# Kernel optimization log

Measured on AMD Instinct MI355X. Metric: run time of the kernel, lower is better.

## Reference

```python
import jax, jax.numpy as jnp
import numpy as np

N_INPUTS = 128
N_LATENT = 21
LEN_TIME = 51
NUM_SHIFTS = 50
BATCH = 2048
N_HIDDEN = 4  # hidden relu layers in the outer DenseResBlock


def setup_inputs() -> dict:
    key = jax.random.key(0)
    ks = jax.random.split(key, 8)
    s = 0.05  # small init scale keeps activations sane through the residual stack
    return {
        "inputs": jax.random.normal(ks[0], (BATCH, LEN_TIME, N_INPUTS), jnp.float32),
        "L": jnp.eye(N_LATENT, dtype=jnp.float32)
             + s * jax.random.normal(ks[1], (N_LATENT, N_LATENT), jnp.float32),
        "ienc_W": s * jax.random.normal(ks[2], (N_INPUTS, N_LATENT), jnp.float32),
        "idec_W": s * jax.random.normal(ks[3], (N_LATENT, N_INPUTS), jnp.float32),
        "enc_W": s * jax.random.normal(ks[4], (N_HIDDEN, N_INPUTS, N_INPUTS), jnp.float32),
        "enc_b": jnp.zeros((N_HIDDEN, N_INPUTS), jnp.float32),
        "enc_Wo": s * jax.random.normal(ks[5], (N_INPUTS, N_INPUTS), jnp.float32),
        "enc_bo": jnp.zeros((N_INPUTS,), jnp.float32),
        "dec_W": s * jax.random.normal(ks[6], (N_HIDDEN, N_INPUTS, N_INPUTS), jnp.float32),
        "dec_b": jnp.zeros((N_HIDDEN, N_INPUTS), jnp.float32),
        "dec_Wo": s * jax.random.normal(ks[7], (N_INPUTS, N_INPUTS), jnp.float32),
        "dec_bo": jnp.zeros((N_INPUTS,), jnp.float32),
    }


def _resblock(x, W, b, Wo, bo):
    # DenseResBlock: stack of relu Dense layers + linear output + residual skip.
    h = x
    for i in range(W.shape[0]):  # fixed small layer count
        h = jax.nn.relu(h @ W[i] + b[i])
    return x + h @ Wo + bo


def reference(inputs, L, ienc_W, idec_W, enc_W, enc_b, enc_Wo, enc_bo,
              dec_W, dec_b, dec_Wo, dec_bo):
    B, T, n_in = inputs.shape
    len_pred = T - NUM_SHIFTS  # = 1

    auto_in = inputs.reshape(-1, n_in)                        # [B*T, n_in]
    pred_in = inputs[:, :len_pred, :].reshape(-1, n_in)       # [B*len_pred, n_in]

    # autoencoder path
    pe = _resblock(auto_in, enc_W, enc_b, enc_Wo, enc_bo)     # partially encoded
    fe = pe @ ienc_W                                          # fully encoded [., n_latent]
    pd = fe @ idec_W                                          # partially decoded
    autoencoder_output = _resblock(pd, dec_W, dec_b, dec_Wo, dec_bo)
    outer_auto_output = _resblock(pe, dec_W, dec_b, dec_Wo, dec_bo)

    # latent rollout: z_{k+1} = z_k @ L, decode every step
    pe_pred = _resblock(pred_in, enc_W, enc_b, enc_Wo, enc_bo)
    z0 = pe_pred @ ienc_W                                     # [B*len_pred, n_latent]

    def step(z, _):
        z_next = z @ L
        return z_next, z_next

    _, zs = jax.lax.scan(step, z0, None, length=NUM_SHIFTS)   # [S, B*len_pred, n_latent]

    # decode all shifts in one large batched pass (same math as per-shift decode)
    dec_in = zs.reshape(-1, zs.shape[-1]) @ idec_W            # [S*B*len_pred, n_in]
    dec_all = _resblock(dec_in, dec_W, dec_b, dec_Wo, dec_bo)
    predictions = (dec_all
                   .reshape(NUM_SHIFTS, B, len_pred, n_in)
                   .transpose(1, 0, 2, 3)
                   .reshape(B, NUM_SHIFTS * len_pred, n_in))

    return autoencoder_output, outer_auto_output, predictions
```

## Files before the change

kernel.cpp:

```cpp
#include <hip/hip_runtime.h>

#define NF 128
#define NLAT 21
#define NBATCH 2048
#define LEN_T 51
#define NSHIFT 50
#define AUTO_ROWS (NBATCH*LEN_T)
#define PRED_ROWS (NBATCH*NSHIFT)

typedef short bh8  __attribute__((ext_vector_type(8)));
typedef unsigned short us8 __attribute__((ext_vector_type(8)));
typedef float f32x4  __attribute__((ext_vector_type(4)));
typedef float f32x16 __attribute__((ext_vector_type(16)));
typedef unsigned u32x4 __attribute__((ext_vector_type(4)));

#define MFMA32(A,B,C) __builtin_amdgcn_mfma_f32_32x32x16_bf16(A,B,C,0,0,0)
#define SGB(m,n) __builtin_amdgcn_sched_group_barrier((m),(n),0)

__device__ __forceinline__ float bf2f(short s){
  unsigned u = ((unsigned)(unsigned short)s) << 16;
  return __builtin_bit_cast(float, u);
}
__device__ __forceinline__ short f2bf(float v){
  unsigned u = __builtin_bit_cast(unsigned, v);
  return (short)((u + 0x7FFFu + ((u>>16)&1u)) >> 16);
}
__device__ __forceinline__ unsigned pk2(float a, float b){
  unsigned ua = __builtin_bit_cast(unsigned, a) + 0x8000u;
  unsigned ub = __builtin_bit_cast(unsigned, b) + 0x8000u;
  return (ua >> 16) | (ub & 0xFFFF0000u);
}

__global__ void k_mmul(const float* __restrict__ ienc, const float* __restrict__ idec,
                       float* __restrict__ M){
  int idx = blockIdx.x*256 + threadIdx.x;
  int i = idx>>7, j = idx&127;
  float s = 0.f;
#pragma unroll
  for(int k=0;k<NLAT;++k) s = fmaf(ienc[i*NLAT+k], idec[k*NF+j], s);
  M[idx] = s;
}

__global__ void k_prep(const float* __restrict__ encW, const float* __restrict__ encWo,
                       const float* __restrict__ decW, const float* __restrict__ decWo,
                       const float* __restrict__ M,    const float* __restrict__ idec,
                       unsigned short* __restrict__ swz){
  int id  = blockIdx.x*256 + threadIdx.x;
  int mat = id >> 11;
  int rem = id & 2047;
  int f   = rem >> 6, l = rem & 63;
  int s   = f >> 2,  mt = f & 3;
  int hl  = l >> 5,  c  = l & 31;
  const float* src;
  if(mat<4)       src = encW + mat*16384;
  else if(mat==4) src = encWo;
  else if(mat<9)  src = decW + (mat-5)*16384;
  else if(mat==9) src = decWo;
  else if(mat==10)src = M;
  else            src = idec;
  us8 w8;
#pragma unroll
  for(int i=0;i<8;++i){
    int k = s*16 + 4*hl + (i&3) + 8*(i>>2);
    float v;
    if(mat==11) v = (k<NLAT) ? src[k*NF + mt*32 + c] : 0.f;
    else        v = src[k*NF + mt*32 + c];
    w8[i] = (unsigned short)f2bf(v);
  }
  *(us8*)(swz + (size_t)mat*16384 + (size_t)f*512 + (size_t)l*8) = w8;
}

__device__ __forceinline__ bh8 ldg8(const unsigned short* p){ return *(const bh8*)p; }

__device__ __forceinline__ void run_half(const unsigned short* __restrict__ wg, int m,
    const bh8 h[8], f32x16 acc[2], int lane){
  f32x16 z;
#pragma unroll
  for(int r=0;r<16;++r) z[r]=0.f;
  acc[0]=z; acc[1]=z;
  const unsigned short* base = wg + m*1024 + lane*8;
  bh8 w0a = ldg8(base);
  bh8 w0b = ldg8(base + 512);
  bh8 w1a = ldg8(base + 2048);
  bh8 w1b = ldg8(base + 2048 + 512);
#pragma unroll
  for(int s=0;s<8;++s){
    bh8 na, nb;
    if(s<6){
      na = ldg8(base + (s+2)*2048);
      nb = ldg8(base + (s+2)*2048 + 512);
      SGB(0x20,2);
    }
    __builtin_amdgcn_s_setprio(1);
    acc[0]=MFMA32(w0a,h[s],acc[0]);
    acc[1]=MFMA32(w0b,h[s],acc[1]);
    __builtin_amdgcn_s_setprio(0);
    SGB(0x8,2);
    if(s<6){ w0a=w1a; w0b=w1b; w1a=na; w1b=nb; }
    else    { w0a=w1a; w0b=w1b; }
  }
}

__device__ __forceinline__ void run_half_k2(const unsigned short* __restrict__ wg, int m,
    const bh8 zf[2], f32x16 acc[2], int lane){
  f32x16 z;
#pragma unroll
  for(int r=0;r<16;++r) z[r]=0.f;
  acc[0]=z; acc[1]=z;
  const unsigned short* base = wg + m*1024 + lane*8;
#pragma unroll
  for(int s=0;s<2;++s){
    bh8 a0 = ldg8(base + s*2048);
    bh8 a1 = ldg8(base + s*2048 + 512);
    acc[0]=MFMA32(a0,zf[s],acc[0]);
    acc[1]=MFMA32(a1,zf[s],acc[1]);
  }
}

__device__ __forceinline__ void epi_hidden_half(const f32x16 acc[2], const float* __restrict__ bl,
    int m, int hl, bh8 out[4]){
#pragma unroll
  for(int t=0;t<2;++t){
    f32x4 b[4];
#pragma unroll
    for(int q=0;q<4;++q) b[q] = *(const f32x4*)(bl + (2*m+t)*32 + q*8 + hl*4);
    f32x16 a = acc[t];
#pragma unroll
    for(int q=0;q<4;++q)
#pragma unroll
      for(int j=0;j<4;++j) a[q*4+j] = fmaxf(a[q*4+j] + b[q][j], 0.f);
#pragma unroll
    for(int p=0;p<2;++p){
      u32x4 w;
#pragma unroll
      for(int j=0;j<4;++j) w[j] = pk2(a[p*8+2*j], a[p*8+2*j+1]);
      out[t*2+p] = __builtin_bit_cast(bh8, w);
    }
  }
}
__device__ __forceinline__ void epi_plain_half(const f32x16 acc[2], bh8 out[4]){
#pragma unroll
  for(int t=0;t<2;++t){
    f32x16 a = acc[t];
#pragma unroll
    for(int p=0;p<2;++p){
      u32x4 w;
#pragma unroll
      for(int j=0;j<4;++j) w[j] = pk2(a[p*8+2*j], a[p*8+2*j+1]);
      out[t*2+p] = __builtin_bit_cast(bh8, w);
    }
  }
}

__device__ __forceinline__ void final_half(float* outp, size_t ro,
    const f32x16 acc[2], const float* __restrict__ bo, const bh8 r4[4], int m, int hl){
#pragma unroll
  for(int t=0;t<2;++t){
    f32x4 b[4];
#pragma unroll
    for(int q=0;q<4;++q) b[q]=*(const f32x4*)(bo + (2*m+t)*32 + q*8 + hl*4);
    f32x16 a = acc[t];
    bh8 r0 = r4[t*2], r1 = r4[t*2+1];
#pragma unroll
    for(int q=0;q<4;++q)
#pragma unroll
      for(int j=0;j<4;++j){
        int r=q*4+j;
        a[r] += b[q][j] + bf2f((r<8 ? r0 : r1)[r&7]);
      }
#pragma unroll
    for(int q=0;q<4;++q){
      f32x4 w; w[0]=a[q*4+0]; w[1]=a[q*4+1]; w[2]=a[q*4+2]; w[3]=a[q*4+3];
      *(f32x4*)(outp + ro + (2*m+t)*32 + q*8 + hl*4) = w;
    }
  }
}

__device__ __forceinline__ void peWo_half(const f32x16 acc[2], const float* __restrict__ bo,
    const bh8 r4[4], int m, int hl, bh8 out[4], float* __restrict__ pe0,
    int bidx, bool isz){
#pragma unroll
  for(int t=0;t<2;++t){
    f32x4 b[4];
#pragma unroll
    for(int q=0;q<4;++q) b[q]=*(const f32x4*)(bo + (2*m+t)*32 + q*8 + hl*4);
    f32x16 a = acc[t];
    bh8 r0 = r4[t*2], r1 = r4[t*2+1];
#pragma unroll
    for(int q=0;q<4;++q)
#pragma unroll
      for(int j=0;j<4;++j){
        int r=q*4+j;
        a[r] += b[q][j] + bf2f((r<8 ? r0 : r1)[r&7]);
      }
    if(isz){
#pragma unroll
      for(int q=0;q<4;++q){
        f32x4 w; w[0]=a[q*4+0]; w[1]=a[q*4+1]; w[2]=a[q*4+2]; w[3]=a[q*4+3];
        *(f32x4*)(pe0 + (size_t)bidx*NF + (2*m+t)*32 + q*8 + hl*4) = w;
      }
    }
#pragma unroll
    for(int p=0;p<2;++p){
      u32x4 w;
#pragma unroll
      for(int j=0;j<4;++j) w[j]=pk2(a[p*8+2*j], a[p*8+2*j+1]);
      out[t*2+p]=__builtin_bit_cast(bh8,w);
    }
  }
}

__device__ __forceinline__ void layer_hidden(const unsigned short* __restrict__ wg,
    const float* __restrict__ bl, bh8 h[8], int lane, int hl){
  f32x16 acc[2]; bh8 t0[4], t1[4];
  run_half(wg,0,h,acc,lane);
  epi_hidden_half(acc,bl,0,hl,t0);
  run_half(wg,1,h,acc,lane);
  epi_hidden_half(acc,bl,1,hl,t1);
#pragma unroll
  for(int k=0;k<4;++k){ h[k]=t0[k]; h[4+k]=t1[k]; }
}

__device__ __forceinline__ void stash8(unsigned short* sp, const bh8 h[8], int lane){
#pragma unroll
  for(int f=0;f<8;++f) *(bh8*)(sp + f*512 + lane*8) = h[f];
}
__device__ __forceinline__ void unstash8f(const unsigned short* sp, bh8 r[8], int lane){
#pragma unroll
  for(int f=0;f<8;++f) r[f] = *(const bh8*)(sp + f*512 + lane*8);
}
__device__ __forceinline__ void unstash4(const unsigned short* sp, bh8 r4[4], int m, int lane){
#pragma unroll
  for(int k=0;k<4;++k) r4[k] = *(const bh8*)(sp + (4*m+k)*512 + lane*8);
}

__global__ __launch_bounds__(64,3)
void k_main5(const float* __restrict__ gin, const unsigned short* __restrict__ swz,
             const float* __restrict__ encB, const float* __restrict__ encBo,
             const float* __restrict__ decB, const float* __restrict__ decBo,
             float* __restrict__ out1, float* __restrict__ out2, float* __restrict__ pe0){
  __shared__ __align__(16) unsigned short sres[4096];
  const int lane = threadIdx.x;
  const int hl = lane>>5, c31 = lane&31;
  const int row = blockIdx.x*32 + c31;
  const size_t ro = (size_t)row*NF;
  const int bidx = row/LEN_T;
  const bool isz = (row == bidx*LEN_T);
  bh8 h[8];

  {
    const float* rp = gin + ro;
#pragma unroll
    for(int s=0;s<8;++s){
      f32x4 a=*(const f32x4*)(rp + s*16 + 4*hl);
      f32x4 b=*(const f32x4*)(rp + s*16 + 8 + 4*hl);
      us8 o;
#pragma unroll
      for(int i=0;i<4;++i){ o[i]=(unsigned short)f2bf(a[i]); o[i+4]=(unsigned short)f2bf(b[i]); }
      h[s]=__builtin_bit_cast(bh8,o);
    }
  }
  stash8(sres, h, lane);

#pragma unroll 1
  for(int l=0;l<4;++l)
    layer_hidden(swz + (size_t)l*16384, encB + l*NF, h, lane, hl);

  {
    const unsigned short* wg = swz + (size_t)4*16384;
    f32x16 acc[2]; bh8 t0[4], t1[4], r4[4];
    run_half(wg,0,h,acc,lane);
    unstash4(sres, r4, 0, lane);
    peWo_half(acc, encBo, r4, 0, hl, t0, pe0, bidx, isz);
    run_half(wg,1,h,acc,lane);
    unstash4(sres, r4, 1, lane);
    peWo_half(acc, encBo, r4, 1, hl, t1, pe0, bidx, isz);
#pragma unroll
    for(int k=0;k<4;++k){ h[k]=t0[k]; h[4+k]=t1[k]; }
    stash8(sres, h, lane);
  }

#pragma unroll 1
  for(int l=0;l<4;++l)
    layer_hidden(swz + (size_t)(5+l)*16384, decB + l*NF, h, lane, hl);

  {
    const unsigned short* wg = swz + (size_t)9*16384;
    f32x16 acc[2]; bh8 r4[4];
    run_half(wg,0,h,acc,lane);
    unstash4(sres, r4, 0, lane);
    final_half(out2, ro, acc, decBo, r4, 0, hl);
    run_half(wg,1,h,acc,lane);
    unstash4(sres, r4, 1, lane);
    final_half(out2, ro, acc, decBo, r4, 1, hl);
  }

  {
    unstash8f(sres, h, lane);
    const unsigned short* wg = swz + (size_t)10*16384;
    f32x16 acc[2]; bh8 t0[4], t1[4];
    run_half(wg,0,h,acc,lane); epi_plain_half(acc,t0);
    run_half(wg,1,h,acc,lane); epi_plain_half(acc,t1);
#pragma unroll
    for(int k=0;k<4;++k){ h[k]=t0[k]; h[4+k]=t1[k]; }
    stash8(sres, h, lane);
  }

#pragma unroll 1
  for(int l=0;l<4;++l)
    layer_hidden(swz + (size_t)(5+l)*16384, decB + l*NF, h, lane, hl);

  {
    const unsigned short* wg = swz + (size_t)9*16384;
    f32x16 acc[2]; bh8 r4[4];
    run_half(wg,0,h,acc,lane);
    unstash4(sres, r4, 0, lane);
    final_half(out1, ro, acc, decBo, r4, 0, hl);
    run_half(wg,1,h,acc,lane);
    unstash4(sres, r4, 1, lane);
    final_half(out1, ro, acc, decBo, r4, 1, hl);
  }
}

__global__ void k_roll(const float* __restrict__ pe0, const float* __restrict__ ienc,
                       const float* __restrict__ L, float* __restrict__ zs){
  const int tid=threadIdx.x, lane=tid&63, wid=tid>>6, sub=lane&31, half=lane>>5;
  const int row=blockIdx.x*8 + wid*2 + half;
  const bool act = sub < NLAT;
  float Lc[NLAT];
#pragma unroll
  for(int k=0;k<NLAT;++k) Lc[k] = act ? L[k*NLAT+sub] : 0.f;
  float z=0.f;
  if(act){
    const float* pr = pe0 + (size_t)row*NF;
    float s0=0.f,s1=0.f,s2=0.f,s3=0.f;
#pragma unroll 8
    for(int k=0;k<NF;k+=4){
      s0=fmaf(pr[k+0], ienc[(k+0)*NLAT+sub], s0);
      s1=fmaf(pr[k+1], ienc[(k+1)*NLAT+sub], s1);
      s2=fmaf(pr[k+2], ienc[(k+2)*NLAT+sub], s2);
      s3=fmaf(pr[k+3], ienc[(k+3)*NLAT+sub], s3);
    }
    z=(s0+s1)+(s2+s3);
  }
  const int base = half*32;
#pragma unroll 1
  for(int s=0;s<NSHIFT;++s){
    float zn=0.f;
#pragma unroll
    for(int k=0;k<NLAT;++k) zn=fmaf(__shfl(z, base+k, 64), Lc[k], zn);
    z=zn;
    if(act) zs[((size_t)s*NBATCH + row)*NLAT + sub] = z;
  }
}

__global__ __launch_bounds__(64,3)
void k_pred5(const float* __restrict__ zs, const unsigned short* __restrict__ swz,
             const float* __restrict__ decB, const float* __restrict__ decBo,
             float* __restrict__ out3){
  __shared__ __align__(16) unsigned short sres[4096];
  const int lane = threadIdx.x;
  const int hl = lane>>5, c31 = lane&31;
  const int prow = blockIdx.x*32 + c31;
  const int orow = (prow & 2047)*NSHIFT + (prow >> 11);
  const size_t oro = (size_t)orow*NF;
  bh8 h[8];

  bh8 zf[2];
  {
    const float* zr = zs + (size_t)prow*NLAT;
#pragma unroll
    for(int s=0;s<2;++s){
      us8 o;
#pragma unroll
      for(int i=0;i<8;++i){
        int cc = s*16 + 4*hl + (i&3) + 8*(i>>2);
        o[i] = (cc<NLAT) ? (unsigned short)f2bf(zr[cc]) : (unsigned short)0;
      }
      zf[s]=__builtin_bit_cast(bh8,o);
    }
  }

  {
    const unsigned short* wg = swz + (size_t)11*16384;
    f32x16 acc[2]; bh8 t0[4], t1[4];
    run_half_k2(wg,0,zf,acc,lane); epi_plain_half(acc,t0);
    run_half_k2(wg,1,zf,acc,lane); epi_plain_half(acc,t1);
#pragma unroll
    for(int k=0;k<4;++k){ h[k]=t0[k]; h[4+k]=t1[k]; }
    stash8(sres, h, lane);
  }

#pragma unroll 1
  for(int l=0;l<4;++l)
    layer_hidden(swz + (size_t)(5+l)*16384, decB + l*NF, h, lane, hl);

  {
    const unsigned short* wg = swz + (size_t)9*16384;
    f32x16 acc[2]; bh8 r4[4];
    run_half(wg,0,h,acc,lane);
    unstash4(sres, r4, 0, lane);
    final_half(out3, oro, acc, decBo, r4, 0, hl);
    run_half(wg,1,h,acc,lane);
    unstash4(sres, r4, 1, lane);
    final_half(out3, oro, acc, decBo, r4, 1, hl);
  }
}

extern "C" void kernel_launch(void* const* d_in, const int* in_sizes, int n_in,
                              void* d_out, int out_size, void* d_ws, size_t ws_size,
                              hipStream_t stream) {
  const float* gin   = (const float*)d_in[0];
  const float* L     = (const float*)d_in[1];
  const float* iencW = (const float*)d_in[2];
  const float* idecW = (const float*)d_in[3];
  const float* encW  = (const float*)d_in[4];
  const float* encB  = (const float*)d_in[5];
  const float* encWo = (const float*)d_in[6];
  const float* encBo = (const float*)d_in[7];
  const float* decW  = (const float*)d_in[8];
  const float* decB  = (const float*)d_in[9];
  const float* decWo = (const float*)d_in[10];
  const float* decBo = (const float*)d_in[11];

  float* out1 = (float*)d_out;
  float* out2 = out1 + (size_t)AUTO_ROWS*NF;
  float* out3 = out2 + (size_t)AUTO_ROWS*NF;

  float* M   = (float*)d_ws;
  float* pe0 = M + 16384;
  float* zs  = pe0 + (size_t)NBATCH*NF;
  unsigned short* swz = (unsigned short*)(zs + (size_t)NSHIFT*NBATCH*NLAT);

  hipLaunchKernelGGL(k_mmul, dim3(64),  dim3(256), 0, stream, iencW, idecW, M);
  hipLaunchKernelGGL(k_prep, dim3(96),  dim3(256), 0, stream, encW, encWo, decW, decWo, M, idecW, swz);
  hipLaunchKernelGGL(k_main5, dim3(AUTO_ROWS/32), dim3(64), 0, stream,
                     gin, swz, encB, encBo, decB, decBo, out1, out2, pe0);
  hipLaunchKernelGGL(k_roll, dim3(NBATCH/8), dim3(256), 0, stream, pe0, iencW, L, zs);
  hipLaunchKernelGGL(k_pred5, dim3(PRED_ROWS/32), dim3(64), 0, stream,
                     zs, swz, decB, decBo, out3);
}
```

Baseline: 190.7 us.

## Stage weights through double-buffered LDS shared by four waves per block

The main and prediction kernels move from one 64-thread wave per block to four waves per block. Each half-weight tile is streamed into a double-buffered LDS area with global_load_lds and shared by all four waves, replacing per-wave global weight loads. Biases are cached in LDS, the residual now lives in registers instead of an LDS stash, and the prep kernel's weight swizzle is reordered to match the contiguous half layout. The aim is to cut repeated L2 weight traffic and improve MFMA feed, at the cost of a block barrier after every half layer and more LDS and registers per block, which can reduce occupancy.

```diff
diff --git a/kernel.cpp b/kernel.cpp
--- a/kernel.cpp
+++ b/kernel.cpp
@@ -15,7 +15,6 @@
 typedef unsigned u32x4 __attribute__((ext_vector_type(4)));
 
 #define MFMA32(A,B,C) __builtin_amdgcn_mfma_f32_32x32x16_bf16(A,B,C,0,0,0)
-#define SGB(m,n) __builtin_amdgcn_sched_group_barrier((m),(n),0)
 
 __device__ __forceinline__ float bf2f(short s){
   unsigned u = ((unsigned)(unsigned short)s) << 16;
@@ -49,7 +48,8 @@
   int mat = id >> 11;
   int rem = id & 2047;
   int f   = rem >> 6, l = rem & 63;
-  int s   = f >> 2,  mt = f & 3;
+  int m   = f >> 4, s = (f >> 1) & 7, t = f & 1;
+  int mt  = 2*m + t;
   int hl  = l >> 5,  c  = l & 31;
   const float* src;
   if(mat<4)       src = encW + mat*16384;
@@ -70,34 +70,31 @@
   *(us8*)(swz + (size_t)mat*16384 + (size_t)f*512 + (size_t)l*8) = w8;
 }
 
-__device__ __forceinline__ bh8 ldg8(const unsigned short* p){ return *(const bh8*)p; }
-
-__device__ __forceinline__ void run_half(const unsigned short* __restrict__ wg, int m,
+__device__ __forceinline__ void stage_half(const unsigned short* g,
+                                           unsigned short* l, int wid, int lane){
+  const unsigned short* gp = g + wid*2048 + lane*8;
+  unsigned short* lp = l + wid*2048;
+#pragma unroll
+  for(int i=0;i<4;++i){
+    __builtin_amdgcn_global_load_lds(
+      (const __attribute__((address_space(1))) void*)(gp + i*512),
+      (__attribute__((address_space(3))) void*)(lp + i*512), 16, 0, 0);
+  }
+}
+
+__device__ __forceinline__ void run_half_lds(const unsigned short* wl,
     const bh8 h[8], f32x16 acc[2], int lane){
   f32x16 z;
 #pragma unroll
   for(int r=0;r<16;++r) z[r]=0.f;
   acc[0]=z; acc[1]=z;
-  const unsigned short* base = wg + m*1024 + lane*8;
-  bh8 w0a = ldg8(base);
-  bh8 w0b = ldg8(base + 512);
-  bh8 w1a = ldg8(base + 2048);
-  bh8 w1b = ldg8(base + 2048 + 512);
+  const unsigned short* base = wl + lane*8;
 #pragma unroll
   for(int s=0;s<8;++s){
-    bh8 na, nb;
-    if(s<6){
-      na = ldg8(base + (s+2)*2048);
-      nb = ldg8(base + (s+2)*2048 + 512);
-      SGB(0x20,2);
-    }
-    __builtin_amdgcn_s_setprio(1);
-    acc[0]=MFMA32(w0a,h[s],acc[0]);
-    acc[1]=MFMA32(w0b,h[s],acc[1]);
-    __builtin_amdgcn_s_setprio(0);
-    SGB(0x8,2);
-    if(s<6){ w0a=w1a; w0b=w1b; w1a=na; w1b=nb; }
-    else    { w0a=w1a; w0b=w1b; }
+    bh8 w0 = *(const bh8*)(base + (2*s)*512);
+    bh8 w1 = *(const bh8*)(base + (2*s+1)*512);
+    acc[0]=MFMA32(w0,h[s],acc[0]);
+    acc[1]=MFMA32(w1,h[s],acc[1]);
   }
 }
 
@@ -107,17 +104,17 @@
 #pragma unroll
   for(int r=0;r<16;++r) z[r]=0.f;
   acc[0]=z; acc[1]=z;
-  const unsigned short* base = wg + m*1024 + lane*8;
+  const unsigned short* base = wg + m*8192 + lane*8;
 #pragma unroll
   for(int s=0;s<2;++s){
-    bh8 a0 = ldg8(base + s*2048);
-    bh8 a1 = ldg8(base + s*2048 + 512);
-    acc[0]=MFMA32(a0,zf[s],acc[0]);
-    acc[1]=MFMA32(a1,zf[s],acc[1]);
-  }
-}
-
-__device__ __forceinline__ void epi_hidden_half(const f32x16 acc[2], const float* __restrict__ bl,
+    bh8 w0 = *(const bh8*)(base + (2*s)*512);
+    bh8 w1 = *(const bh8*)(base + (2*s+1)*512);
+    acc[0]=MFMA32(w0,zf[s],acc[0]);
+    acc[1]=MFMA32(w1,zf[s],acc[1]);
+  }
+}
+
+__device__ __forceinline__ void epi_hidden_half(const f32x16 acc[2], const float* bl,
     int m, int hl, bh8 out[4]){
 #pragma unroll
   for(int t=0;t<2;++t){
@@ -151,16 +148,15 @@
     }
   }
 }
-
 __device__ __forceinline__ void final_half(float* outp, size_t ro,
-    const f32x16 acc[2], const float* __restrict__ bo, const bh8 r4[4], int m, int hl){
+    const f32x16 acc[2], const float* bo, const bh8 res8[8], int m, int hl){
 #pragma unroll
   for(int t=0;t<2;++t){
     f32x4 b[4];
 #pragma unroll
     for(int q=0;q<4;++q) b[q]=*(const f32x4*)(bo + (2*m+t)*32 + q*8 + hl*4);
     f32x16 a = acc[t];
-    bh8 r0 = r4[t*2], r1 = r4[t*2+1];
+    bh8 r0 = res8[4*m+2*t], r1 = res8[4*m+2*t+1];
 #pragma unroll
     for(int q=0;q<4;++q)
 #pragma unroll
@@ -175,9 +171,8 @@
     }
   }
 }
-
-__device__ __forceinline__ void peWo_half(const f32x16 acc[2], const float* __restrict__ bo,
-    const bh8 r4[4], int m, int hl, bh8 out[4], float* __restrict__ pe0,
+__device__ __forceinline__ void peWo_half(const f32x16 acc[2], const float* bo,
+    const bh8 res8[8], int m, int hl, bh8 out[4], float* __restrict__ pe0,
     int bidx, bool isz){
 #pragma unroll
   for(int t=0;t<2;++t){
@@ -185,7 +180,7 @@
 #pragma unroll
     for(int q=0;q<4;++q) b[q]=*(const f32x4*)(bo + (2*m+t)*32 + q*8 + hl*4);
     f32x16 a = acc[t];
-    bh8 r0 = r4[t*2], r1 = r4[t*2+1];
+    bh8 r0 = res8[4*m+2*t], r1 = res8[4*m+2*t+1];
 #pragma unroll
     for(int q=0;q<4;++q)
 #pragma unroll
@@ -210,44 +205,25 @@
   }
 }
 
-__device__ __forceinline__ void layer_hidden(const unsigned short* __restrict__ wg,
-    const float* __restrict__ bl, bh8 h[8], int lane, int hl){
-  f32x16 acc[2]; bh8 t0[4], t1[4];
-  run_half(wg,0,h,acc,lane);
-  epi_hidden_half(acc,bl,0,hl,t0);
-  run_half(wg,1,h,acc,lane);
-  epi_hidden_half(acc,bl,1,hl,t1);
-#pragma unroll
-  for(int k=0;k<4;++k){ h[k]=t0[k]; h[4+k]=t1[k]; }
-}
-
-__device__ __forceinline__ void stash8(unsigned short* sp, const bh8 h[8], int lane){
-#pragma unroll
-  for(int f=0;f<8;++f) *(bh8*)(sp + f*512 + lane*8) = h[f];
-}
-__device__ __forceinline__ void unstash8f(const unsigned short* sp, bh8 r[8], int lane){
-#pragma unroll
-  for(int f=0;f<8;++f) r[f] = *(const bh8*)(sp + f*512 + lane*8);
-}
-__device__ __forceinline__ void unstash4(const unsigned short* sp, bh8 r4[4], int m, int lane){
-#pragma unroll
-  for(int k=0;k<4;++k) r4[k] = *(const bh8*)(sp + (4*m+k)*512 + lane*8);
-}
-
-__global__ __launch_bounds__(64,3)
-void k_main5(const float* __restrict__ gin, const unsigned short* __restrict__ swz,
+__global__ __launch_bounds__(256,3)
+void k_main6(const float* __restrict__ gin, const unsigned short* __restrict__ swz,
              const float* __restrict__ encB, const float* __restrict__ encBo,
              const float* __restrict__ decB, const float* __restrict__ decBo,
              float* __restrict__ out1, float* __restrict__ out2, float* __restrict__ pe0){
-  __shared__ __align__(16) unsigned short sres[4096];
-  const int lane = threadIdx.x;
-  const int hl = lane>>5, c31 = lane&31;
-  const int row = blockIdx.x*32 + c31;
+  __shared__ __align__(16) unsigned short wb[2][8192];
+  __shared__ __align__(16) float blds[1280];
+  const int tid=threadIdx.x, lane=tid&63, wid=tid>>6;
+  const int hl=lane>>5, c31=lane&31;
+  const int row = blockIdx.x*128 + wid*32 + c31;
   const size_t ro = (size_t)row*NF;
   const int bidx = row/LEN_T;
   const bool isz = (row == bidx*LEN_T);
-  bh8 h[8];
-
+  bh8 h[8], res[8], t0[4], t1[4];
+  f32x16 acc[2];
+
+  stage_half(swz, wb[0], wid, lane);
+  for(int i=tid;i<1280;i+=256)
+    blds[i] = (i<512)?encB[i] : (i<1024)?decB[i-512] : (i<1152)?encBo[i-1024] : decBo[i-1152];
   {
     const float* rp = gin + ro;
 #pragma unroll
@@ -258,67 +234,94 @@
 #pragma unroll
       for(int i=0;i<4;++i){ o[i]=(unsigned short)f2bf(a[i]); o[i+4]=(unsigned short)f2bf(b[i]); }
       h[s]=__builtin_bit_cast(bh8,o);
-    }
-  }
-  stash8(sres, h, lane);
+      res[s]=h[s];
+    }
+  }
+  __syncthreads();
+  int cur=0;
 
 #pragma unroll 1
-  for(int l=0;l<4;++l)
-    layer_hidden(swz + (size_t)l*16384, encB + l*NF, h, lane, hl);
-
-  {
-    const unsigned short* wg = swz + (size_t)4*16384;
-    f32x16 acc[2]; bh8 t0[4], t1[4], r4[4];
-    run_half(wg,0,h,acc,lane);
-    unstash4(sres, r4, 0, lane);
-    peWo_half(acc, encBo, r4, 0, hl, t0, pe0, bidx, isz);
-    run_half(wg,1,h,acc,lane);
-    unstash4(sres, r4, 1, lane);
-    peWo_half(acc, encBo, r4, 1, hl, t1, pe0, bidx, isz);
+  for(int l=0;l<4;++l){
+    stage_half(swz + (size_t)l*16384 + 8192, wb[cur^1], wid, lane);
+    run_half_lds(wb[cur], h, acc, lane);
+    epi_hidden_half(acc, blds + l*NF, 0, hl, t0);
+    __syncthreads(); cur^=1;
+    stage_half(swz + (size_t)(l+1)*16384, wb[cur^1], wid, lane);
+    run_half_lds(wb[cur], h, acc, lane);
+    epi_hidden_half(acc, blds + l*NF, 1, hl, t1);
+    __syncthreads(); cur^=1;
 #pragma unroll
     for(int k=0;k<4;++k){ h[k]=t0[k]; h[4+k]=t1[k]; }
-    stash8(sres, h, lane);
-  }
-
+  }
+  {
+    stage_half(swz + (size_t)4*16384 + 8192, wb[cur^1], wid, lane);
+    run_half_lds(wb[cur], h, acc, lane);
+    peWo_half(acc, blds+1024, res, 0, hl, t0, pe0, bidx, isz);
+    __syncthreads(); cur^=1;
+    stage_half(swz + (size_t)5*16384, wb[cur^1], wid, lane);
+    run_half_lds(wb[cur], h, acc, lane);
+    peWo_half(acc, blds+1024, res, 1, hl, t1, pe0, bidx, isz);
+    __syncthreads(); cur^=1;
+#pragma unroll
+    for(int k=0;k<4;++k){ h[k]=t0[k]; h[4+k]=t1[k]; res[k]=t0[k]; res[4+k]=t1[k]; }
+  }
 #pragma unroll 1
-  for(int l=0;l<4;++l)
-    layer_hidden(swz + (size_t)(5+l)*16384, decB + l*NF, h, lane, hl);
-
-  {
-    const unsigned short* wg = swz + (size_t)9*16384;
-    f32x16 acc[2]; bh8 r4[4];
-    run_half(wg,0,h,acc,lane);
-    unstash4(sres, r4, 0, lane);
-    final_half(out2, ro, acc, decBo, r4, 0, hl);
-    run_half(wg,1,h,acc,lane);
-    unstash4(sres, r4, 1, lane);
-    final_half(out2, ro, acc, decBo, r4, 1, hl);
-  }
-
-  {
-    unstash8f(sres, h, lane);
-    const unsigned short* wg = swz + (size_t)10*16384;
-    f32x16 acc[2]; bh8 t0[4], t1[4];
-    run_half(wg,0,h,acc,lane); epi_plain_half(acc,t0);
-    run_half(wg,1,h,acc,lane); epi_plain_half(acc,t1);
+  for(int l=0;l<4;++l){
+    stage_half(swz + (size_t)(5+l)*16384 + 8192, wb[cur^1], wid, lane);
+    run_half_lds(wb[cur], h, acc, lane);
+    epi_hidden_half(acc, blds + 512 + l*NF, 0, hl, t0);
+    __syncthreads(); cur^=1;
+    stage_half(swz + (size_t)(6+l)*16384, wb[cur^1], wid, lane);
+    run_half_lds(wb[cur], h, acc, lane);
+    epi_hidden_half(acc, blds + 512 + l*NF, 1, hl, t1);
+    __syncthreads(); cur^=1;
 #pragma unroll
     for(int k=0;k<4;++k){ h[k]=t0[k]; h[4+k]=t1[k]; }
-    stash8(sres, h, lane);
-  }
-
+  }
+  {
+    stage_half(swz + (size_t)9*16384 + 8192, wb[cur^1], wid, lane);
+    run_half_lds(wb[cur], h, acc, lane);
+    final_half(out2, ro, acc, blds+1152, res, 0, hl);
+    __syncthreads(); cur^=1;
+    stage_half(swz + (size_t)10*16384, wb[cur^1], wid, lane);
+    run_half_lds(wb[cur], h, acc, lane);
+    final_half(out2, ro, acc, blds+1152, res, 1, hl);
+    __syncthreads(); cur^=1;
+  }
+  {
+#pragma unroll
+    for(int k=0;k<8;++k) h[k]=res[k];
+    stage_half(swz + (size_t)10*16384 + 8192, wb[cur^1], wid, lane);
+    run_half_lds(wb[cur], h, acc, lane);
+    epi_plain_half(acc, t0);
+    __syncthreads(); cur^=1;
+    stage_half(swz + (size_t)5*16384, wb[cur^1], wid, lane);
+    run_half_lds(wb[cur], h, acc, lane);
+    epi_plain_half(acc, t1);
+    __syncthreads(); cur^=1;
+#pragma unroll
+    for(int k=0;k<4;++k){ h[k]=t0[k]; h[4+k]=t1[k]; res[k]=t0[k]; res[4+k]=t1[k]; }
+  }
 #pragma unroll 1
-  for(int l=0;l<4;++l)
-    layer_hidden(swz + (size_t)(5+l)*16384, decB + l*NF, h, lane, hl);
-
-  {
-    const unsigned short* wg = swz + (size_t)9*16384;
-    f32x16 acc[2]; bh8 r4[4];
-    run_half(wg,0,h,acc,lane);
-    unstash4(sres, r4, 0, lane);
-    final_half(out1, ro, acc, decBo, r4, 0, hl);
-    run_half(wg,1,h,acc,lane);
-    unstash4(sres, r4, 1, lane);
-    final_half(out1, ro, acc, decBo, r4, 1, hl);
+  for(int l=0;l<4;++l){
+    stage_half(swz + (size_t)(5+l)*16384 + 8192, wb[cur^1], wid, lane);
+    run_half_lds(wb[cur], h, acc, lane);
+    epi_hidden_half(acc, blds + 512 + l*NF, 0, hl, t0);
+    __syncthreads(); cur^=1;
+    stage_half(swz + (size_t)(6+l)*16384, wb[cur^1], wid, lane);
+    run_half_lds(wb[cur], h, acc, lane);
+    epi_hidden_half(acc, blds + 512 + l*NF, 1, hl, t1);
+    __syncthreads(); cur^=1;
+#pragma unroll
+    for(int k=0;k<4;++k){ h[k]=t0[k]; h[4+k]=t1[k]; }
+  }
+  {
+    stage_half(swz + (size_t)9*16384 + 8192, wb[cur^1], wid, lane);
+    run_half_lds(wb[cur], h, acc, lane);
+    final_half(out1, ro, acc, blds+1152, res, 0, hl);
+    __syncthreads(); cur^=1;
+    run_half_lds(wb[cur], h, acc, lane);
+    final_half(out1, ro, acc, blds+1152, res, 1, hl);
   }
 }
 
@@ -354,17 +357,22 @@
   }
 }
 
-__global__ __launch_bounds__(64,3)
-void k_pred5(const float* __restrict__ zs, const unsigned short* __restrict__ swz,
+__global__ __launch_bounds__(256,3)
+void k_pred6(const float* __restrict__ zs, const unsigned short* __restrict__ swz,
              const float* __restrict__ decB, const float* __restrict__ decBo,
              float* __restrict__ out3){
-  __shared__ __align__(16) unsigned short sres[4096];
-  const int lane = threadIdx.x;
-  const int hl = lane>>5, c31 = lane&31;
-  const int prow = blockIdx.x*32 + c31;
+  __shared__ __align__(16) unsigned short wb[2][8192];
+  __shared__ __align__(16) float blds[640];
+  const int tid=threadIdx.x, lane=tid&63, wid=tid>>6;
+  const int hl=lane>>5, c31=lane&31;
+  const int prow = blockIdx.x*128 + wid*32 + c31;
   const int orow = (prow & 2047)*NSHIFT + (prow >> 11);
   const size_t oro = (size_t)orow*NF;
-  bh8 h[8];
+  bh8 h[8], res[8], t0[4], t1[4];
+  f32x16 acc[2];
+
+  stage_half(swz + (size_t)5*16384, wb[0], wid, lane);
+  for(int i=tid;i<640;i+=256) blds[i] = (i<512) ? decB[i] : decBo[i-512];
 
   bh8 zf[2];
   {
@@ -380,30 +388,36 @@
       zf[s]=__builtin_bit_cast(bh8,o);
     }
   }
-
   {
     const unsigned short* wg = swz + (size_t)11*16384;
-    f32x16 acc[2]; bh8 t0[4], t1[4];
-    run_half_k2(wg,0,zf,acc,lane); epi_plain_half(acc,t0);
-    run_half_k2(wg,1,zf,acc,lane); epi_plain_half(acc,t1);
+    run_half_k2(wg, 0, zf, acc, lane); epi_plain_half(acc, t0);
+    run_half_k2(wg, 1, zf, acc, lane); epi_plain_half(acc, t1);
+#pragma unroll
+    for(int k=0;k<4;++k){ h[k]=t0[k]; h[4+k]=t1[k]; res[k]=t0[k]; res[4+k]=t1[k]; }
+  }
+  __syncthreads();
+  int cur=0;
+
+#pragma unroll 1
+  for(int l=0;l<4;++l){
+    stage_half(swz + (size_t)(5+l)*16384 + 8192, wb[cur^1], wid, lane);
+    run_half_lds(wb[cur], h, acc, lane);
+    epi_hidden_half(acc, blds + l*NF, 0, hl, t0);
+    __syncthreads(); cur^=1;
+    stage_half(swz + (size_t)(6+l)*16384, wb[cur^1], wid, lane);
+    run_half_lds(wb[cur], h, acc, lane);
+    epi_hidden_half(acc, blds + l*NF, 1, hl, t1);
+    __syncthreads(); cur^=1;
 #pragma unroll
     for(int k=0;k<4;++k){ h[k]=t0[k]; h[4+k]=t1[k]; }
-    stash8(sres, h, lane);
-  }
-
-#pragma unroll 1
-  for(int l=0;l<4;++l)
-    layer_hidden(swz + (size_t)(5+l)*16384, decB + l*NF, h, lane, hl);
-
-  {
-    const unsigned short* wg = swz + (size_t)9*16384;
-    f32x16 acc[2]; bh8 r4[4];
-    run_half(wg,0,h,acc,lane);
-    unstash4(sres, r4, 0, lane);
-    final_half(out3, oro, acc, decBo, r4, 0, hl);
-    run_half(wg,1,h,acc,lane);
-    unstash4(sres, r4, 1, lane);
-    final_half(out3, oro, acc, decBo, r4, 1, hl);
+  }
+  {
+    stage_half(swz + (size_t)9*16384 + 8192, wb[cur^1], wid, lane);
+    run_half_lds(wb[cur], h, acc, lane);
+    final_half(out3, oro, acc, blds+512, res, 0, hl);
+    __syncthreads(); cur^=1;
+    run_half_lds(wb[cur], h, acc, lane);
+    final_half(out3, oro, acc, blds+512, res, 1, hl);
   }
 }
 
@@ -434,9 +448,9 @@
 
   hipLaunchKernelGGL(k_mmul, dim3(64),  dim3(256), 0, stream, iencW, idecW, M);
   hipLaunchKernelGGL(k_prep, dim3(96),  dim3(256), 0, stream, encW, encWo, decW, decWo, M, idecW, swz);
-  hipLaunchKernelGGL(k_main5, dim3(AUTO_ROWS/32), dim3(64), 0, stream,
+  hipLaunchKernelGGL(k_main6, dim3(AUTO_ROWS/128), dim3(256), 0, stream,
                      gin, swz, encB, encBo, decB, decBo, out1, out2, pe0);
   hipLaunchKernelGGL(k_roll, dim3(NBATCH/8), dim3(256), 0, stream, pe0, iencW, L, zs);
-  hipLaunchKernelGGL(k_pred5, dim3(PRED_ROWS/32), dim3(64), 0, stream,
+  hipLaunchKernelGGL(k_pred6, dim3(PRED_ROWS/128), dim3(256), 0, stream,
                      zs, swz, decB, decBo, out3);
 }
```

After: 164.6 us. 13.7% less time.
